# Performance work log

Measured on AMD Instinct MI355X. Metric: run time of the kernel, lower is better.

Reference implementation:

```python
import jax, jax.numpy as jnp
import numpy as np

N = 100000      # input points
NS = 12500      # sampled points (fps ratio=0.125)
E = 400000      # edges (~32 neighbors per sampled point)
F_IN = 64       # down_conv_nn[0]
HID = 32        # in_features // 2 (pre_mlp output, PointKernel width)
F_OUT = 128     # down_conv_nn[1]
K = 16          # num kernel points
RADIUS = 1.0
KP_EXTENT = RADIUS / 1.5


def setup_inputs() -> dict:
    key = jax.random.key(0)
    ks = jax.random.split(key, 14)
    x = jax.random.normal(ks[0], (N, F_IN), dtype=jnp.float32)
    pos = jax.random.uniform(ks[1], (N, 3), dtype=jnp.float32, minval=-1.0, maxval=1.0)
    idx = jnp.sort(jax.random.randint(ks[2], (NS,), 0, N))
    edge_src = jax.random.randint(ks[3], (E,), 0, N)    # col: source / full cloud
    edge_dst = jax.random.randint(ks[4], (E,), 0, NS)   # row: target / sampled cloud
    # kernel point positions (stand-in for kernel_point_optimization_debug output)
    kernel = jax.random.uniform(ks[5], (K, 3), dtype=jnp.float32, minval=-RADIUS, maxval=RADIUS)
    # per-kernel-point weight matrices
    kernel_weight = jax.random.normal(ks[6], (K, HID, HID), dtype=jnp.float32) * (1.0 / np.sqrt(HID))
    pre_W = jax.random.normal(ks[7], (F_IN, HID), dtype=jnp.float32) * (1.0 / np.sqrt(F_IN))
    pre_b = jax.random.normal(ks[8], (HID,), dtype=jnp.float32) * 0.01
    post_W = jax.random.normal(ks[9], (HID, F_OUT), dtype=jnp.float32) * (1.0 / np.sqrt(HID))
    post_b = jax.random.normal(ks[10], (F_OUT,), dtype=jnp.float32) * 0.01
    short_W = jax.random.normal(ks[11], (F_IN, F_OUT), dtype=jnp.float32) * (1.0 / np.sqrt(F_IN))
    short_b = jax.random.normal(ks[12], (F_OUT,), dtype=jnp.float32) * 0.01
    return {
        "x": x, "pos": pos,
        "pre_W": pre_W, "pre_b": pre_b,
        "kernel": kernel, "kernel_weight": kernel_weight,
        "post_W": post_W, "post_b": post_b,
        "short_W": short_W, "short_b": short_b,
        "idx": idx, "edge_src": edge_src, "edge_dst": edge_dst,
    }


def reference(x, pos, pre_W, pre_b, kernel, kernel_weight,
              post_W, post_b, short_W, short_b,
              idx, edge_src, edge_dst):
    # pre MLP on full cloud features
    x_side = x @ pre_W + pre_b                      # [N, HID]
    pos_sub = pos[idx]                              # [NS, 3]

    # message: per-edge relative position
    neighbors = pos[edge_src] - pos_sub[edge_dst]   # [E, 3]
    differences = neighbors[:, None, :] - kernel[None, :, :]  # [E, K, 3]
    sq_distances = jnp.sum(differences * differences, axis=-1)  # [E, K]

    # linear KP influence, clipped at 0
    all_weights = jnp.maximum(1.0 - sq_distances / (KP_EXTENT ** 2), 0.0)
    nn1 = jnp.argmin(sq_distances, axis=-1)         # [E] nearest kernel point
    w = jnp.take_along_axis(all_weights, nn1[:, None], axis=1)  # [E, 1]

    K_weights = kernel_weight[nn1]                  # [E, HID, HID] big gather
    weighted_features = w * x_side[edge_src]        # einsum('nb,nc->nc') with b==1
    msg = jnp.einsum('na,nac->nc', weighted_features, K_weights)  # [E, HID]

    # scatter-add aggregation over target nodes
    agg = jax.ops.segment_sum(msg, edge_dst, num_segments=NS)      # [NS, HID]

    out_side = agg @ post_W + post_b                # [NS, F_OUT]
    out_short = x[idx] @ short_W + short_b          # [NS, F_OUT]
    return out_side + out_short
```

## Files before the change

### kernel.cpp

```cpp
#include <hip/hip_runtime.h>

#define F_IN   64
#define HID    32
#define F_OUT  128
#define KPTS   16
#define CAP    80
#define INV_EXT2 2.25f

__global__ __launch_bounds__(256) void k1_pre(
    const float* __restrict__ x, const float* __restrict__ pre_W,
    const float* __restrict__ pre_b, const float* __restrict__ pos,
    const int* __restrict__ idx,
    float* __restrict__ x_side, float* __restrict__ pos_sub,
    int* __restrict__ cursor, int N, int NS)
{
    const int gt = blockIdx.x * 256 + threadIdx.x;
    const int gstride = gridDim.x * 256;

    for (int i = gt; i < NS; i += gstride) cursor[i] = 0;
    for (int i = gt; i < NS * 3; i += gstride) {
        int r = i / 3, c = i - r * 3;
        pos_sub[i] = pos[(long long)idx[r] * 3 + c];
    }

    const int c = threadIdx.x & 31;
    float wcol[F_IN];
#pragma unroll
    for (int a = 0; a < F_IN; ++a) wcol[a] = pre_W[a * HID + c];
    const float bias = pre_b[c];

    const int group   = blockIdx.x * 8 + (threadIdx.x >> 5);
    const int ngroups = gridDim.x * 8;
    for (int row = group; row < N; row += ngroups) {
        const float4* xr = (const float4*)(x + (long long)row * F_IN);
        float acc = bias;
#pragma unroll
        for (int q = 0; q < 16; ++q) {
            const float4 xv = xr[q];
            acc = fmaf(xv.x, wcol[4 * q + 0], acc);
            acc = fmaf(xv.y, wcol[4 * q + 1], acc);
            acc = fmaf(xv.z, wcol[4 * q + 2], acc);
            acc = fmaf(xv.w, wcol[4 * q + 3], acc);
        }
        x_side[(long long)row * HID + c] = acc;
    }
}

__global__ __launch_bounds__(256) void k2_prep(
    const float* __restrict__ pos, const float* __restrict__ pos_sub,
    const float* __restrict__ kp,
    const int* __restrict__ edge_src, const int* __restrict__ edge_dst,
    int* __restrict__ cursor, uint2* __restrict__ pkw, int E)
{
    __shared__ float skp[KPTS * 3];
    if (threadIdx.x < KPTS * 3) skp[threadIdx.x] = kp[threadIdx.x];
    __syncthreads();

    for (int t = blockIdx.x * 256 + threadIdx.x; t < E; t += gridDim.x * 256) {
        const int src = edge_src[t];
        const int dst = edge_dst[t];
        const float nx = pos[src * 3 + 0] - pos_sub[dst * 3 + 0];
        const float ny = pos[src * 3 + 1] - pos_sub[dst * 3 + 1];
        const float nz = pos[src * 3 + 2] - pos_sub[dst * 3 + 2];

        float best = 1e30f;
        int   nn   = 0;
#pragma unroll
        for (int k = 0; k < KPTS; ++k) {
            const float dx = nx - skp[k * 3 + 0];
            const float dy = ny - skp[k * 3 + 1];
            const float dz = nz - skp[k * 3 + 2];
            const float sq = dx * dx + dy * dy + dz * dz;
            if (sq < best) { best = sq; nn = k; }
        }
        const float w = fmaxf(1.0f - best * INV_EXT2, 0.0f);

        const int slot = atomicAdd(&cursor[dst], 1);
        if (slot < CAP)
            pkw[(long long)dst * CAP + slot] =
                make_uint2((unsigned)src | ((unsigned)nn << 20), __float_as_uint(w));
    }
}

__global__ __launch_bounds__(256, 4) void k3_agg(
    const uint2* __restrict__ pkw, const int* __restrict__ cursor,
    const float* __restrict__ x_side, const float* __restrict__ kw,
    float* __restrict__ agg, int NS, int N)
{
    __shared__ float s_lds[8 * KPTS * HID];
    __shared__ float part[8 * 8 * HID];

    const int l = threadIdx.x & 31;
    const int g = threadIdx.x >> 5;
    const int d = blockIdx.x * 8 + g;

    float kwreg[64];
#pragma unroll
    for (int j = 0; j < 64; ++j)
        kwreg[j] = kw[(g * 64 + j) * HID + l];

    float4* s4 = (float4*)s_lds;
#pragma unroll
    for (int i = 0; i < 4; ++i)
        s4[i * 256 + threadIdx.x] = make_float4(0.f, 0.f, 0.f, 0.f);
    __syncthreads();

    float* sg = s_lds + g * (KPTS * HID);

    int cnt = 0;
    if (d < NS) {
        cnt = cursor[d];
        if (cnt > CAP) cnt = CAP;
    }
    const uint2* bp = pkw + (long long)(d < NS ? d : 0) * CAP;

    uint2 e0 = bp[0], e1 = bp[1], e2 = bp[2];
    unsigned s0 = e0.x & 0xFFFFFu; if (s0 >= (unsigned)N) s0 = 0;
    unsigned s1 = e1.x & 0xFFFFFu; if (s1 >= (unsigned)N) s1 = 0;
    float xs0 = x_side[s0 * HID + l];
    float xs1 = x_side[s1 * HID + l];

    for (int i = 0; i < cnt; ++i) {
        const uint2 e3 = bp[i + 3];
        unsigned s2 = e2.x & 0xFFFFFu; if (s2 >= (unsigned)N) s2 = 0;
        const float xs2 = x_side[s2 * HID + l];

        const float wf = __uint_as_float(e0.y) * xs0;
        const int   nn = (int)(e0.x >> 20);
        __hip_atomic_fetch_add(&sg[nn * HID + l], wf,
                               __ATOMIC_RELAXED, __HIP_MEMORY_SCOPE_WORKGROUP);

        e0 = e1; e1 = e2; e2 = e3;
        xs0 = xs1; xs1 = xs2;
    }
    __syncthreads();

    float pacc[8];
#pragma unroll
    for (int dd = 0; dd < 8; ++dd) {
        const float4* srow = (const float4*)(s_lds + dd * (KPTS * HID) + g * 64);
        float acc = 0.f;
#pragma unroll
        for (int q = 0; q < 16; ++q) {
            const float4 sv = srow[q];
            acc = fmaf(sv.x, kwreg[4 * q + 0], acc);
            acc = fmaf(sv.y, kwreg[4 * q + 1], acc);
            acc = fmaf(sv.z, kwreg[4 * q + 2], acc);
            acc = fmaf(sv.w, kwreg[4 * q + 3], acc);
        }
        pacc[dd] = acc;
    }

#pragma unroll
    for (int dd = 0; dd < 8; ++dd)
        part[(dd * 8 + g) * HID + l] = pacc[dd];
    __syncthreads();

    if (d < NS) {
        float r = 0.f;
#pragma unroll
        for (int j = 0; j < 8; ++j)
            r += part[(g * 8 + j) * HID + l];
        agg[(long long)d * HID + l] = r;
    }
}

__global__ __launch_bounds__(128) void k4_out(
    const float* __restrict__ agg,
    const float* __restrict__ post_W, const float* __restrict__ post_b,
    const float* __restrict__ x,
    const float* __restrict__ short_W, const float* __restrict__ short_b,
    const int* __restrict__ idx, float* __restrict__ out, int NS)
{
    const int c = threadIdx.x;
    float pw[HID];
#pragma unroll
    for (int a = 0; a < HID; ++a) pw[a] = post_W[a * F_OUT + c];
    float sw[F_IN];
#pragma unroll
    for (int b = 0; b < F_IN; ++b) sw[b] = short_W[b * F_OUT + c];
    const float bias = post_b[c] + short_b[c];

    for (int r = blockIdx.x; r < NS; r += gridDim.x) {
        const float4* ar = (const float4*)(agg + (long long)r * HID);
        const float4* xr = (const float4*)(x + (long long)idx[r] * F_IN);
        float acc = bias;
#pragma unroll
        for (int q = 0; q < 8; ++q) {
            const float4 v = ar[q];
            acc = fmaf(v.x, pw[4 * q + 0], acc);
            acc = fmaf(v.y, pw[4 * q + 1], acc);
            acc = fmaf(v.z, pw[4 * q + 2], acc);
            acc = fmaf(v.w, pw[4 * q + 3], acc);
        }
#pragma unroll
        for (int q = 0; q < 16; ++q) {
            const float4 v = xr[q];
            acc = fmaf(v.x, sw[4 * q + 0], acc);
            acc = fmaf(v.y, sw[4 * q + 1], acc);
            acc = fmaf(v.z, sw[4 * q + 2], acc);
            acc = fmaf(v.w, sw[4 * q + 3], acc);
        }
        out[(long long)r * F_OUT + c] = acc;
    }
}

extern "C" void kernel_launch(void* const* d_in, const int* in_sizes, int n_in,
                              void* d_out, int out_size, void* d_ws, size_t ws_size,
                              hipStream_t stream)
{
    const float* x        = (const float*)d_in[0];
    const float* pos      = (const float*)d_in[1];
    const float* pre_W    = (const float*)d_in[2];
    const float* pre_b    = (const float*)d_in[3];
    const float* kp       = (const float*)d_in[4];
    const float* kweight  = (const float*)d_in[5];
    const float* post_W   = (const float*)d_in[6];
    const float* post_b   = (const float*)d_in[7];
    const float* short_W  = (const float*)d_in[8];
    const float* short_b  = (const float*)d_in[9];
    const int*   idx      = (const int*)d_in[10];
    const int*   edge_src = (const int*)d_in[11];
    const int*   edge_dst = (const int*)d_in[12];
    float*       out      = (float*)d_out;

    const int N  = in_sizes[0] / F_IN;
    const int NS = in_sizes[10];
    const int E  = in_sizes[11];

    char* ws = (char*)d_ws;
    size_t off = 0;
    auto alloc = [&](size_t bytes) {
        void* p = ws + off;
        off = (off + bytes + 255) & ~(size_t)255;
        return p;
    };
    float* x_side  = (float*) alloc((size_t)N * HID * 4);
    float* pos_sub = (float*) alloc((size_t)NS * 3 * 4);
    int*   cursor  = (int*)   alloc((size_t)NS * 4);
    uint2* pkw     = (uint2*) alloc(((size_t)NS * CAP + 32) * 8);
    float* agg     = (float*) alloc((size_t)NS * HID * 4);

    k1_pre<<<1536, 256, 0, stream>>>(x, pre_W, pre_b, pos, idx,
                                     x_side, pos_sub, cursor, N, NS);
    k2_prep<<<(E + 255) / 256, 256, 0, stream>>>(pos, pos_sub, kp,
                                                 edge_src, edge_dst,
                                                 cursor, pkw, E);
    k3_agg<<<(NS + 7) / 8, 256, 0, stream>>>(pkw, cursor, x_side,
                                             kweight, agg, NS, N);
    k4_out<<<2048, 128, 0, stream>>>(agg, post_W, post_b, x,
                                     short_W, short_b, idx, out, NS);
}
```

Before: 176.2 us.

## Batch-prefetch eight edges per step in aggregation loop and raise occupancy

The per-edge gather loop in k3_agg now loads edges and their x_side values in batches of eight, double-buffered, instead of a three-deep rolling prefetch. This puts more independent global loads in flight to hide gather latency. The 64-register kernel-weight preload is moved after the loop so it no longer holds registers during the gather phase, and the launch bound is raised from 4 to 6 blocks per CU. In exchange, the loop uses more registers for the buffers and reads up to eight entries past each destination row's filled slots.

```diff
diff --git a/kernel.cpp b/kernel.cpp
--- a/kernel.cpp
+++ b/kernel.cpp
@@ -82,7 +82,7 @@
     }
 }
 
-__global__ __launch_bounds__(256, 4) void k3_agg(
+__global__ __launch_bounds__(256, 6) void k3_agg(
     const uint2* __restrict__ pkw, const int* __restrict__ cursor,
     const float* __restrict__ x_side, const float* __restrict__ kw,
     float* __restrict__ agg, int NS, int N)
@@ -93,11 +93,6 @@
     const int l = threadIdx.x & 31;
     const int g = threadIdx.x >> 5;
     const int d = blockIdx.x * 8 + g;
-
-    float kwreg[64];
-#pragma unroll
-    for (int j = 0; j < 64; ++j)
-        kwreg[j] = kw[(g * 64 + j) * HID + l];
 
     float4* s4 = (float4*)s_lds;
 #pragma unroll
@@ -114,25 +109,43 @@
     }
     const uint2* bp = pkw + (long long)(d < NS ? d : 0) * CAP;
 
-    uint2 e0 = bp[0], e1 = bp[1], e2 = bp[2];
-    unsigned s0 = e0.x & 0xFFFFFu; if (s0 >= (unsigned)N) s0 = 0;
-    unsigned s1 = e1.x & 0xFFFFFu; if (s1 >= (unsigned)N) s1 = 0;
-    float xs0 = x_side[s0 * HID + l];
-    float xs1 = x_side[s1 * HID + l];
-
-    for (int i = 0; i < cnt; ++i) {
-        const uint2 e3 = bp[i + 3];
-        unsigned s2 = e2.x & 0xFFFFFu; if (s2 >= (unsigned)N) s2 = 0;
-        const float xs2 = x_side[s2 * HID + l];
-
-        const float wf = __uint_as_float(e0.y) * xs0;
-        const int   nn = (int)(e0.x >> 20);
-        __hip_atomic_fetch_add(&sg[nn * HID + l], wf,
-                               __ATOMIC_RELAXED, __HIP_MEMORY_SCOPE_WORKGROUP);
-
-        e0 = e1; e1 = e2; e2 = e3;
-        xs0 = xs1; xs1 = xs2;
-    }
+    uint2 eA[8]; float xsA[8];
+#pragma unroll
+    for (int j = 0; j < 8; ++j) eA[j] = bp[j];
+#pragma unroll
+    for (int j = 0; j < 8; ++j) {
+        unsigned s = eA[j].x & 0xFFFFFu; if (s >= (unsigned)N) s = 0;
+        xsA[j] = x_side[s * HID + l];
+    }
+
+    for (int i0 = 0; i0 < cnt; i0 += 8) {
+        uint2 eB[8]; float xsB[8];
+#pragma unroll
+        for (int j = 0; j < 8; ++j) eB[j] = bp[i0 + 8 + j];
+#pragma unroll
+        for (int j = 0; j < 8; ++j) {
+            unsigned s = eB[j].x & 0xFFFFFu; if (s >= (unsigned)N) s = 0;
+            xsB[j] = x_side[s * HID + l];
+        }
+#pragma unroll
+        for (int j = 0; j < 8; ++j) {
+            if (i0 + j < cnt) {
+                const float wf = __uint_as_float(eA[j].y) * xsA[j];
+                const int   nn = (int)(eA[j].x >> 20);
+                __hip_atomic_fetch_add(&sg[nn * HID + l], wf,
+                                       __ATOMIC_RELAXED,
+                                       __HIP_MEMORY_SCOPE_WORKGROUP);
+            }
+        }
+#pragma unroll
+        for (int j = 0; j < 8; ++j) { eA[j] = eB[j]; xsA[j] = xsB[j]; }
+    }
+
+    float kwreg[64];
+#pragma unroll
+    for (int j = 0; j < 64; ++j)
+        kwreg[j] = kw[(g * 64 + j) * HID + l];
+
     __syncthreads();
 
     float pacc[8];
```

Result: faster. 167.7 us (-4.8%).
